# Optimization experiments

Measured on AMD Instinct MI355X. Metric: run time of the kernel, lower is better.

Reference implementation:

```python
import jax, jax.numpy as jnp
import numpy as np
from jax import lax

B, S, H = 64, 512, 768
L = 20          # num_labels
MAX_SPANS = 8   # span_number_classifier has MAX_SPANS+1 outputs


def setup_inputs() -> dict:
    key = jax.random.key(0)
    k = jax.random.split(key, 8)
    w = lambda i, shape: jax.random.normal(k[i], shape, jnp.float32) * 0.02
    return {
        "tokens_rep": jax.random.normal(k[0], (B, S, H), jnp.float32),
        "seq_rep": jax.random.normal(k[1], (B, H), jnp.float32),
        "w_start": w(2, (H,)), "b_start": jnp.zeros((), jnp.float32),
        "w_end": w(3, (H,)), "b_end": jnp.zeros((), jnp.float32),
        "W_nspans": w(4, (H, MAX_SPANS + 1)), "b_nspans": jnp.zeros((MAX_SPANS + 1,), jnp.float32),
        "W_span": w(5, (H, L)), "b_span": jnp.zeros((L,), jnp.float32),
        "W_pol": w(6, (H + L, L)), "b_pol": jnp.zeros((L,), jnp.float32),
    }


def _select_spans(ss, es, n_spans):
    """Faithful port of get_top_spans_nongreedy's while-loop.
    ss/es: [MAX_SPANS] ascending-sorted top indices (sentinel S beyond n_spans).
    Each iteration advances s_idx and/or e_idx, so 2*MAX_SPANS steps suffice."""
    def body(i, st):
        s_idx, e_idx, last_end, rem, out_s, out_e, cnt = st
        active = (rem > 0) & (s_idx < n_spans) & (e_idx < n_spans)
        s = ss[jnp.minimum(s_idx, MAX_SPANS - 1)]
        e = es[jnp.minimum(e_idx, MAX_SPANS - 1)]
        accept = active & (e > s) & (s >= last_end)
        inc_e = active & (~accept) & (e <= s)
        inc_s = active & (~accept) & (e > s)
        out_s = jnp.where(accept, out_s.at[cnt].set(s), out_s)
        out_e = jnp.where(accept, out_e.at[cnt].set(e), out_e)
        last_end = jnp.where(accept, e, last_end)
        a = accept.astype(jnp.int32)
        return (s_idx + a + inc_s.astype(jnp.int32),
                e_idx + a + inc_e.astype(jnp.int32),
                last_end, rem - a, out_s, out_e, cnt + a)

    z = jnp.zeros((MAX_SPANS,), jnp.int32)
    init = (jnp.int32(0), jnp.int32(0), jnp.int32(0), n_spans, z, z, jnp.int32(0))
    st = lax.fori_loop(0, 2 * MAX_SPANS, body, init)
    return st[4], st[5], st[6]  # starts, ends, count


def _per_item(tokens, starts, ends, fsl, n_spans, W_span, b_span):
    # sigmoid is monotone, so top-k of sigmoid(logits) == top-k of logits
    _, i_s = lax.top_k(starts, MAX_SPANS)
    _, i_e = lax.top_k(ends, MAX_SPANS)
    rank = jnp.arange(MAX_SPANS)
    keep = rank < n_spans
    ss = jnp.sort(jnp.where(keep, i_s, S).astype(jnp.int32))  # sentinel S sorts last
    es = jnp.sort(jnp.where(keep, i_e, S).astype(jnp.int32))
    out_s, out_e, cnt = _select_spans(ss, es, n_spans)
    valid = rank < cnt
    vf = valid.astype(tokens.dtype)

    # span mean-pooling tokens[s:e+1].mean(0) via a [MAX_SPANS,S] mask matmul
    t = jnp.arange(S)
    span_mask = ((t[None, :] >= out_s[:, None]) & (t[None, :] <= out_e[:, None])).astype(tokens.dtype)
    lengths = (out_e - out_s + 1).astype(tokens.dtype)
    span_vecs = (span_mask @ tokens) / lengths[:, None]         # [MAX_SPANS, H]

    mls = jax.nn.softmax(span_vecs @ W_span + b_span, axis=1)   # [MAX_SPANS, L]
    span_labels = jnp.argmax(mls, axis=1)
    fsl_soft = jax.nn.softmax(fsl)
    has_valid = cnt > 0

    labels_oh_m = jnp.zeros((L,), tokens.dtype).at[span_labels].max(vf)
    labels_oh_m = jnp.where(has_valid, labels_oh_m,
                            jnp.zeros((L,), tokens.dtype).at[jnp.argmax(fsl_soft)].set(1.0))
    spans_m = jnp.max(jnp.where(valid[:, None], mls, -jnp.inf), axis=0)
    spans_m = jnp.where(has_valid, spans_m, jnp.zeros((L,), tokens.dtype))
    starts_oh_m = jnp.zeros((S,), tokens.dtype).at[out_s].max(vf)
    ends_oh_m = jnp.zeros((S,), tokens.dtype).at[out_e].max(vf)

    # n_spans <= 1 branch
    labels_oh_1 = jnp.zeros((L,), tokens.dtype).at[jnp.argmax(fsl_soft)].set(1.0)
    starts_oh_1 = jnp.zeros((S,), tokens.dtype).at[jnp.argmax(starts)].set(1.0)
    ends_oh_1 = jnp.zeros((S,), tokens.dtype).at[jnp.argmax(ends)].set(1.0)

    single = n_spans <= 1
    spans = jnp.where(single, fsl_soft, spans_m)
    labels_oh = jnp.where(single, labels_oh_1, labels_oh_m)
    starts_oh = jnp.where(single, starts_oh_1, starts_oh_m)
    ends_oh = jnp.where(single, ends_oh_1, ends_oh_m)
    return spans, starts_oh, ends_oh, labels_oh


def reference(tokens_rep, seq_rep, w_start, b_start, w_end, b_end,
              W_nspans, b_nspans, W_span, b_span, W_pol, b_pol):
    full_seq_logits = seq_rep @ W_span + b_span        # [B, L]
    start_logits = tokens_rep @ w_start + b_start      # [B, S]
    end_logits = tokens_rep @ w_end + b_end            # [B, S]
    n_spans_logits = seq_rep @ W_nspans + b_nspans     # [B, MAX_SPANS+1]
    all_n_spans = jnp.argmax(n_spans_logits, axis=1).astype(jnp.int32)

    spans, starts_oh, ends_oh, labels_oh = jax.vmap(
        _per_item, in_axes=(0, 0, 0, 0, 0, None, None)
    )(tokens_rep, start_logits, end_logits, full_seq_logits, all_n_spans, W_span, b_span)

    pol_logits = jnp.concatenate([seq_rep, spans], axis=1) @ W_pol + b_pol
    return (start_logits, end_logits, spans, n_spans_logits, pol_logits,
            starts_oh, ends_oh, labels_oh)
```

## Files before the change

### kernel.cpp

```cpp
#include <hip/hip_runtime.h>
#include <math.h>

#define NB 64
#define SS 512
#define HH 768
#define LL 20
#define MS 8
#define NSPC 9

#define OFF_START 0
#define OFF_END   (NB*SS)
#define OFF_SPANS (2*NB*SS)
#define OFF_NSP   (2*NB*SS + NB*LL)
#define OFF_POL   (2*NB*SS + NB*LL + NB*NSPC)
#define OFF_SOH   (2*NB*SS + 2*NB*LL + NB*NSPC)
#define OFF_EOH   (3*NB*SS + 2*NB*LL + NB*NSPC)
#define OFF_LOH   (4*NB*SS + 2*NB*LL + NB*NSPC)

struct WS {
  float fsl[NB][LL];
  float mls[NB][MS][LL];
  int   nspans[NB];
  int   fslarg[NB];
  int   cnt[NB];
  int   out_s[NB][MS];
  int   out_e[NB][MS];
  int   slabel[NB][MS];
};

__global__ __launch_bounds__(256) void kA(
    const float4* __restrict__ tok,
    const float* __restrict__ wstart, const float* __restrict__ bstart,
    const float* __restrict__ wend,  const float* __restrict__ bend,
    const float* __restrict__ seq,
    const float* __restrict__ Wspan, const float* __restrict__ bspan,
    const float* __restrict__ Wnsp,  const float* __restrict__ bnsp,
    float* __restrict__ out, WS* __restrict__ ws)
{
  int t = threadIdx.x;
  int wave = t >> 6, lane = t & 63;

  if (blockIdx.x < 1024) {
    __shared__ float4 shs[HH/4], she[HH/4];
    const float4* wsg = (const float4*)wstart;
    const float4* weg = (const float4*)wend;
    for (int i = t; i < HH/4; i += 256) { shs[i] = wsg[i]; she[i] = weg[i]; }
    __syncthreads();
    int r0 = blockIdx.x * 32 + wave * 8;
    const float4* base = tok + (size_t)r0 * (HH/4);
    float as[8] = {0.f,0.f,0.f,0.f,0.f,0.f,0.f,0.f};
    float ae[8] = {0.f,0.f,0.f,0.f,0.f,0.f,0.f,0.f};
    #pragma unroll
    for (int k = 0; k < 3; ++k) {
      int idx = k*64 + lane;
      float4 a = shs[idx], c = she[idx];
      #pragma unroll
      for (int j = 0; j < 8; ++j) {
        float4 x = base[(size_t)j * (HH/4) + idx];
        as[j] += x.x*a.x + x.y*a.y + x.z*a.z + x.w*a.w;
        ae[j] += x.x*c.x + x.y*c.y + x.z*c.z + x.w*c.w;
      }
    }
    float b0 = bstart[0], b1 = bend[0];
    #pragma unroll
    for (int j = 0; j < 8; ++j) {
      float a = as[j], e = ae[j];
      for (int off = 32; off >= 1; off >>= 1) { a += __shfl_down(a, off); e += __shfl_down(e, off); }
      if (lane == 0) {
        out[OFF_START + r0 + j] = a + b0;
        out[OFF_END   + r0 + j] = e + b1;
      }
    }
  } else {
    int b = blockIdx.x - 1024;
    __shared__ float sh[HH];
    __shared__ float logits[LL + NSPC];
    for (int i = t; i < HH; i += 256) sh[i] = seq[b*HH + i];
    __syncthreads();
    for (int o = wave; o < LL + NSPC; o += 4) {
      float acc = 0.f;
      if (o < LL) {
        for (int k = 0; k < HH/64; ++k) { int h = lane + 64*k; acc += sh[h] * Wspan[h*LL + o]; }
      } else {
        int j = o - LL;
        for (int k = 0; k < HH/64; ++k) { int h = lane + 64*k; acc += sh[h] * Wnsp[h*NSPC + j]; }
      }
      for (int off = 32; off >= 1; off >>= 1) acc += __shfl_down(acc, off);
      if (lane == 0) logits[o] = acc + (o < LL ? bspan[o] : bnsp[o - LL]);
    }
    __syncthreads();
    if (t == 0) {
      int bi = 0; float bv = logits[LL];
      #pragma unroll
      for (int j = 1; j < NSPC; ++j) { float v = logits[LL + j]; if (v > bv) { bv = v; bi = j; } }
      ws->nspans[b] = bi;
      int fi = 0; float fv = logits[0];
      #pragma unroll
      for (int j = 1; j < LL; ++j) { float v = logits[j]; if (v > fv) { fv = v; fi = j; } }
      ws->fslarg[b] = fi;
    }
    if (t < LL)  ws->fsl[b][t] = logits[t];
    if (t < NSPC) out[OFF_NSP + b*NSPC + t] = logits[LL + t];
  }
}

__global__ __launch_bounds__(256) void kB(
    float* __restrict__ out, WS* __restrict__ ws)
{
  int b = blockIdx.x;
  int t = threadIdx.x;
  int wave = t >> 6, lane = t & 63;

  __shared__ float candV[2][32];
  __shared__ int   candI[2][32];
  __shared__ int   topI[2][MS];
  __shared__ int   sh_cnt, sh_single;
  __shared__ int   sh_os[MS], sh_oe[MS];

  float sv0 = out[OFF_START + b*SS + t];
  float sv1 = out[OFF_START + b*SS + t + 256];
  float ev0 = out[OFF_END   + b*SS + t];
  float ev1 = out[OFF_END   + b*SS + t + 256];
  int   si0 = t, si1 = t + 256, ei0 = t, ei1 = t + 256;

  #pragma unroll
  for (int k = 0; k < MS; ++k) {
    float lvS = sv0; int liS = si0;
    if (sv1 > lvS) { lvS = sv1; liS = si1; }
    float lvE = ev0; int liE = ei0;
    if (ev1 > lvE) { lvE = ev1; liE = ei1; }
    #pragma unroll
    for (int m = 32; m >= 1; m >>= 1) {
      float ovS = __shfl_xor(lvS, m); int oiS = __shfl_xor(liS, m);
      if (ovS > lvS || (ovS == lvS && oiS < liS)) { lvS = ovS; liS = oiS; }
      float ovE = __shfl_xor(lvE, m); int oiE = __shfl_xor(liE, m);
      if (ovE > lvE || (ovE == lvE && oiE < liE)) { lvE = ovE; liE = oiE; }
    }
    if (lane == 0) {
      candV[0][wave*MS + k] = lvS; candI[0][wave*MS + k] = liS;
      candV[1][wave*MS + k] = lvE; candI[1][wave*MS + k] = liE;
    }
    if (si0 == liS) sv0 = -INFINITY;
    if (si1 == liS) sv1 = -INFINITY;
    if (ei0 == liE) ev0 = -INFINITY;
    if (ei1 == liE) ev1 = -INFINITY;
  }
  __syncthreads();

  if (wave < 2) {
    float v = -INFINITY; int idx = 0x7fffffff;
    if (lane < 32) { v = candV[wave][lane]; idx = candI[wave][lane]; }
    int rank = 0;
    #pragma unroll
    for (int j = 0; j < 32; ++j) {
      float vj = __shfl(v, j); int ij = __shfl(idx, j);
      if (vj > v || (vj == v && ij < idx)) ++rank;
    }
    if (lane < 32 && rank < MS) topI[wave][rank] = idx;
  }
  __syncthreads();

  if (wave == 0) {
    int n = ws->nspans[b];
    int xs = SS, xe = SS;
    if (lane < MS && lane < n) { xs = topI[0][lane]; xe = topI[1][lane]; }
    int rs = 0, re = 0;
    #pragma unroll
    for (int j = 0; j < MS; ++j) {
      int xj = __shfl(xs, j);
      if (xj < xs || (xj == xs && j < lane)) ++rs;
      int yj = __shfl(xe, j);
      if (yj < xe || (yj == xe && j < lane)) ++re;
    }
    int ss_srt = 0, es_srt = 0;
    #pragma unroll
    for (int j = 0; j < MS; ++j) {
      int xj = __shfl(xs, j); int rj = __shfl(rs, j);
      if (rj == lane) ss_srt = xj;
      int yj = __shfl(xe, j); int qj = __shfl(re, j);
      if (qj == lane) es_srt = yj;
    }
    int si = 0, ei = 0, last = 0, rem = n, cnt = 0;
    int my_os = 0, my_oe = 0;
    for (int it = 0; it < 2*MS; ++it) {
      bool active = (rem > 0) && (si < n) && (ei < n);
      int s = __shfl(ss_srt, si < MS ? si : MS - 1);
      int e = __shfl(es_srt, ei < MS ? ei : MS - 1);
      bool accept = active && (e > s) && (s >= last);
      bool ince = active && !accept && (e <= s);
      bool incs = active && !accept && (e > s);
      if (accept) {
        if (lane == cnt) { my_os = s; my_oe = e; }
        last = e; ++cnt; --rem; ++si; ++ei;
      } else {
        si += incs ? 1 : 0; ei += ince ? 1 : 0;
      }
    }
    if (lane < MS) {
      sh_os[lane] = my_os; sh_oe[lane] = my_oe;
      ws->out_s[b][lane] = my_os; ws->out_e[b][lane] = my_oe;
    }
    if (lane == 0) {
      sh_cnt = cnt; sh_single = (n <= 1) ? 1 : 0;
      ws->cnt[b] = cnt;
    }
  }
  __syncthreads();

  int cnt = sh_cnt, single = sh_single;
  for (int pos = t; pos < SS; pos += 256) {
    float sval = 0.f, eval = 0.f;
    if (single) {
      if (pos == topI[0][0]) sval = 1.f;
      if (pos == topI[1][0]) eval = 1.f;
    } else {
      for (int i = 0; i < cnt; ++i) {
        if (pos == sh_os[i]) sval = 1.f;
        if (pos == sh_oe[i]) eval = 1.f;
      }
    }
    out[OFF_SOH + b*SS + pos] = sval;
    out[OFF_EOH + b*SS + pos] = eval;
  }
}

__global__ __launch_bounds__(1024) void kC(
    const float4* __restrict__ tok,
    const float* __restrict__ Wspan, const float* __restrict__ bspan,
    WS* __restrict__ ws)
{
  int b = blockIdx.x >> 3;
  int i = blockIdx.x & (MS - 1);
  if (i >= ws->cnt[b]) return;
  int s0 = ws->out_s[b][i], e0 = ws->out_e[b][i];
  int t = threadIdx.x;
  int g = t >> 8;
  int tid = t & 255;

  __shared__ float4 part[4][HH/4];
  __shared__ float pooled[HH];
  __shared__ float lg[LL];

  if (tid < HH/4) {
    float4 acc = make_float4(0.f, 0.f, 0.f, 0.f);
    const float4* base = tok + (size_t)b * SS * (HH/4) + tid;
    #pragma unroll 4
    for (int r = s0 + g; r <= e0; r += 4) {
      float4 x = base[(size_t)r * (HH/4)];
      acc.x += x.x; acc.y += x.y; acc.z += x.z; acc.w += x.w;
    }
    part[g][tid] = acc;
  }
  __syncthreads();

  if (t < HH/4) {
    float4 p0 = part[0][t], p1 = part[1][t], p2 = part[2][t], p3 = part[3][t];
    float inv = 1.f / (float)(e0 - s0 + 1);
    float4 s;
    s.x = (p0.x + p1.x + p2.x + p3.x) * inv;
    s.y = (p0.y + p1.y + p2.y + p3.y) * inv;
    s.z = (p0.z + p1.z + p2.z + p3.z) * inv;
    s.w = (p0.w + p1.w + p2.w + p3.w) * inv;
    ((float4*)pooled)[t] = s;
  }
  __syncthreads();

  int wave = t >> 6, lane = t & 63;
  for (int l = wave; l < LL; l += 16) {
    float acc = 0.f;
    for (int k = 0; k < HH/64; ++k) { int h = lane + 64*k; acc += pooled[h] * Wspan[h*LL + l]; }
    for (int off = 32; off >= 1; off >>= 1) acc += __shfl_down(acc, off);
    if (lane == 0) lg[l] = acc + bspan[l];
  }
  __syncthreads();

  if (t == 0) {
    float v[LL]; float mx = -INFINITY;
    #pragma unroll
    for (int l = 0; l < LL; ++l) { v[l] = lg[l]; mx = fmaxf(mx, v[l]); }
    int am = 0; float av = v[0];
    #pragma unroll
    for (int l = 1; l < LL; ++l) if (v[l] > av) { av = v[l]; am = l; }
    float sum = 0.f;
    #pragma unroll
    for (int l = 0; l < LL; ++l) { v[l] = expf(v[l] - mx); sum += v[l]; }
    float isum = 1.f / sum;
    #pragma unroll
    for (int l = 0; l < LL; ++l) ws->mls[b][i][l] = v[l] * isum;
    ws->slabel[b][i] = am;
  }
}

__global__ __launch_bounds__(256) void kD(
    const float* __restrict__ seq,
    const float* __restrict__ Wpol, const float* __restrict__ bpol,
    float* __restrict__ out, WS* __restrict__ ws)
{
  int b = blockIdx.x;
  int t = threadIdx.x;
  __shared__ float sp[LL];
  __shared__ float fsl_soft[LL];
  int n = ws->nspans[b];
  int single = (n <= 1) ? 1 : 0;
  int cnt = ws->cnt[b];
  int fa = ws->fslarg[b];
  if (t == 0) {
    float lg[LL]; float mx = -INFINITY;
    #pragma unroll
    for (int l = 0; l < LL; ++l) { lg[l] = ws->fsl[b][l]; mx = fmaxf(mx, lg[l]); }
    float sum = 0.f;
    #pragma unroll
    for (int l = 0; l < LL; ++l) { lg[l] = expf(lg[l] - mx); sum += lg[l]; }
    float isum = 1.f / sum;
    #pragma unroll
    for (int l = 0; l < LL; ++l) fsl_soft[l] = lg[l] * isum;
  }
  __syncthreads();
  if (t < LL) {
    float v;
    if (single) v = fsl_soft[t];
    else if (cnt > 0) { v = -INFINITY; for (int i = 0; i < cnt; ++i) v = fmaxf(v, ws->mls[b][i][t]); }
    else v = 0.f;
    sp[t] = v;
    out[OFF_SPANS + b*LL + t] = v;
    float lo = 0.f;
    if (single || cnt == 0) lo = (t == fa) ? 1.f : 0.f;
    else { for (int i = 0; i < cnt; ++i) if (ws->slabel[b][i] == t) lo = 1.f; }
    out[OFF_LOH + b*LL + t] = lo;
  }
  __syncthreads();
  int wave = t >> 6, lane = t & 63;
  const float* seqb = seq + b*HH;
  for (int l = wave; l < LL; l += 4) {
    float acc = 0.f;
    for (int k = 0; k < 13; ++k) {
      int h = lane + 64*k;
      if (h < HH + LL) {
        float v = (h < HH) ? seqb[h] : sp[h - HH];
        acc += v * Wpol[h*LL + l];
      }
    }
    for (int off = 32; off >= 1; off >>= 1) acc += __shfl_down(acc, off);
    if (lane == 0) out[OFF_POL + b*LL + l] = acc + bpol[l];
  }
}

extern "C" void kernel_launch(void* const* d_in, const int* in_sizes, int n_in,
                              void* d_out, int out_size, void* d_ws, size_t ws_size,
                              hipStream_t stream)
{
  const float* tok    = (const float*)d_in[0];
  const float* seq    = (const float*)d_in[1];
  const float* wstart = (const float*)d_in[2];
  const float* bstart = (const float*)d_in[3];
  const float* wend   = (const float*)d_in[4];
  const float* bend   = (const float*)d_in[5];
  const float* Wnsp   = (const float*)d_in[6];
  const float* bnsp   = (const float*)d_in[7];
  const float* Wspan  = (const float*)d_in[8];
  const float* bspan  = (const float*)d_in[9];
  const float* Wpol   = (const float*)d_in[10];
  const float* bpol   = (const float*)d_in[11];
  float* out = (float*)d_out;
  WS* ws = (WS*)d_ws;

  kA<<<1088, 256, 0, stream>>>((const float4*)tok, wstart, bstart, wend, bend,
                               seq, Wspan, bspan, Wnsp, bnsp, out, ws);
  kB<<<NB, 256, 0, stream>>>(out, ws);
  kC<<<NB*MS, 1024, 0, stream>>>((const float4*)tok, Wspan, bspan, ws);
  kD<<<NB, 256, 0, stream>>>(seq, Wpol, bpol, out, ws);
}
```

Baseline: 84.99 us.

## Move per-block top-8 candidate selection into the logits kernel

Each kA block now ranks its 32 start and end logits and writes its local top-8 candidates with indices to workspace. kB then merges 16×8 candidates per batch instead of re-reading all 512 logits and running the full two-level top-k. This shifts reduction work into kA, where it overlaps with the memory-bound dot products, and shortens the serial kB. It adds a __syncthreads and shuffle ranking to every kA block, plus extra workspace traffic. The output loop is also unrolled.

```diff
diff --git a/kernel.cpp b/kernel.cpp
--- a/kernel.cpp
+++ b/kernel.cpp
@@ -26,6 +26,10 @@
   int   out_s[NB][MS];
   int   out_e[NB][MS];
   int   slabel[NB][MS];
+  float candSV[NB][16][MS];
+  int   candSI[NB][16][MS];
+  float candEV[NB][16][MS];
+  int   candEI[NB][16][MS];
 };
 
 __global__ __launch_bounds__(256) void kA(
@@ -41,7 +45,10 @@
   int wave = t >> 6, lane = t & 63;
 
   if (blockIdx.x < 1024) {
+    int b = blockIdx.x >> 4;
+    int blk = blockIdx.x & 15;
     __shared__ float4 shs[HH/4], she[HH/4];
+    __shared__ float lvS[32], lvE[32];
     const float4* wsg = (const float4*)wstart;
     const float4* weg = (const float4*)wend;
     for (int i = t; i < HH/4; i += 256) { shs[i] = wsg[i]; she[i] = weg[i]; }
@@ -69,6 +76,26 @@
       if (lane == 0) {
         out[OFF_START + r0 + j] = a + b0;
         out[OFF_END   + r0 + j] = e + b1;
+        int slot = wave*8 + j;
+        lvS[slot] = a + b0; lvE[slot] = e + b1;
+      }
+    }
+    __syncthreads();
+    if (wave < 2) {
+      float v = -INFINITY; int idx = 0x7fffffff;
+      if (lane < 32) {
+        v = wave ? lvE[lane] : lvS[lane];
+        idx = blk*32 + lane;
+      }
+      int rank = 0;
+      #pragma unroll
+      for (int j = 0; j < 32; ++j) {
+        float vj = __shfl(v, j); int ij = __shfl(idx, j);
+        if (vj > v || (vj == v && ij < idx)) ++rank;
+      }
+      if (lane < 32 && rank < MS) {
+        if (wave == 0) { ws->candSV[b][blk][rank] = v; ws->candSI[b][blk][rank] = idx; }
+        else           { ws->candEV[b][blk][rank] = v; ws->candEI[b][blk][rank] = idx; }
       }
     }
   } else {
@@ -111,52 +138,28 @@
   int t = threadIdx.x;
   int wave = t >> 6, lane = t & 63;
 
-  __shared__ float candV[2][32];
-  __shared__ int   candI[2][32];
-  __shared__ int   topI[2][MS];
-  __shared__ int   sh_cnt, sh_single;
-  __shared__ int   sh_os[MS], sh_oe[MS];
-
-  float sv0 = out[OFF_START + b*SS + t];
-  float sv1 = out[OFF_START + b*SS + t + 256];
-  float ev0 = out[OFF_END   + b*SS + t];
-  float ev1 = out[OFF_END   + b*SS + t + 256];
-  int   si0 = t, si1 = t + 256, ei0 = t, ei1 = t + 256;
-
-  #pragma unroll
-  for (int k = 0; k < MS; ++k) {
-    float lvS = sv0; int liS = si0;
-    if (sv1 > lvS) { lvS = sv1; liS = si1; }
-    float lvE = ev0; int liE = ei0;
-    if (ev1 > lvE) { lvE = ev1; liE = ei1; }
-    #pragma unroll
-    for (int m = 32; m >= 1; m >>= 1) {
-      float ovS = __shfl_xor(lvS, m); int oiS = __shfl_xor(liS, m);
-      if (ovS > lvS || (ovS == lvS && oiS < liS)) { lvS = ovS; liS = oiS; }
-      float ovE = __shfl_xor(lvE, m); int oiE = __shfl_xor(liE, m);
-      if (ovE > lvE || (ovE == lvE && oiE < liE)) { lvE = ovE; liE = oiE; }
-    }
-    if (lane == 0) {
-      candV[0][wave*MS + k] = lvS; candI[0][wave*MS + k] = liS;
-      candV[1][wave*MS + k] = lvE; candI[1][wave*MS + k] = liE;
-    }
-    if (si0 == liS) sv0 = -INFINITY;
-    if (si1 == liS) sv1 = -INFINITY;
-    if (ei0 == liE) ev0 = -INFINITY;
-    if (ei1 == liE) ev1 = -INFINITY;
-  }
-  __syncthreads();
+  __shared__ int topI[2][MS];
+  __shared__ int sh_cnt, sh_single;
+  __shared__ int sh_os[MS], sh_oe[MS];
 
   if (wave < 2) {
-    float v = -INFINITY; int idx = 0x7fffffff;
-    if (lane < 32) { v = candV[wave][lane]; idx = candI[wave][lane]; }
-    int rank = 0;
-    #pragma unroll
-    for (int j = 0; j < 32; ++j) {
-      float vj = __shfl(v, j); int ij = __shfl(idx, j);
-      if (vj > v || (vj == v && ij < idx)) ++rank;
-    }
-    if (lane < 32 && rank < MS) topI[wave][rank] = idx;
+    const float* cv = wave ? &ws->candEV[b][0][0] : &ws->candSV[b][0][0];
+    const int*   ci = wave ? &ws->candEI[b][0][0] : &ws->candSI[b][0][0];
+    float c0v = cv[lane], c1v = cv[lane + 64];
+    int   c0i = ci[lane], c1i = ci[lane + 64];
+    #pragma unroll
+    for (int k = 0; k < MS; ++k) {
+      float lv = c0v; int li = c0i;
+      if (c1v > lv || (c1v == lv && c1i < li)) { lv = c1v; li = c1i; }
+      #pragma unroll
+      for (int m = 32; m >= 1; m >>= 1) {
+        float ov = __shfl_xor(lv, m); int oi = __shfl_xor(li, m);
+        if (ov > lv || (ov == lv && oi < li)) { lv = ov; li = oi; }
+      }
+      if (lane == 0) topI[wave][k] = li;
+      if (c0i == li) c0v = -INFINITY;
+      if (c1i == li) c1v = -INFINITY;
+    }
   }
   __syncthreads();
 
@@ -201,14 +204,16 @@
       ws->out_s[b][lane] = my_os; ws->out_e[b][lane] = my_oe;
     }
     if (lane == 0) {
-      sh_cnt = cnt; sh_single = (n <= 1) ? 1 : 0;
+      sh_cnt = cnt; sh_single = (ws->nspans[b] <= 1) ? 1 : 0;
       ws->cnt[b] = cnt;
     }
   }
   __syncthreads();
 
   int cnt = sh_cnt, single = sh_single;
-  for (int pos = t; pos < SS; pos += 256) {
+  #pragma unroll
+  for (int pp = 0; pp < 2; ++pp) {
+    int pos = t + pp * 256;
     float sval = 0.f, eval = 0.f;
     if (single) {
       if (pos == topI[0][0]) sval = 1.f;
```

After: 79.58 us. -6.4%, faster.
